# Performance work log

Hardware: AMD Instinct MI355X
Metric: run time of the kernel (lower is better)

Reference implementation:

```python
import jax, jax.numpy as jnp
import numpy as np

D_MODEL = 1024
H = 16
D_K = D_MODEL // H
D_FF = 4096
EPS = 1e-6
NEG = -1.0e9


def setup_inputs() -> dict:
    key = jax.random.key(0)
    ks = jax.random.split(key, 8)
    B, S = 4, 2048
    x = jax.random.normal(ks[0], (B, S, D_MODEL), dtype=jnp.float32)
    src_mask = jnp.ones((B, 1, S, S), dtype=jnp.int32)
    s = 0.02
    wq = jax.random.normal(ks[1], (D_MODEL, D_MODEL), jnp.float32) * s
    wk = jax.random.normal(ks[2], (D_MODEL, D_MODEL), jnp.float32) * s
    wv = jax.random.normal(ks[3], (D_MODEL, D_MODEL), jnp.float32) * s
    wo = jax.random.normal(ks[4], (D_MODEL, D_MODEL), jnp.float32) * s
    w1 = jax.random.normal(ks[5], (D_MODEL, D_FF), jnp.float32) * s
    b1 = jnp.zeros((D_FF,), jnp.float32)
    w2 = jax.random.normal(ks[6], (D_FF, D_MODEL), jnp.float32) * s
    b2 = jnp.zeros((D_MODEL,), jnp.float32)
    # LayerNorm params are scalars in the original (torch.ones(1)/zeros(1))
    a1 = jnp.ones((1,), jnp.float32); bt1 = jnp.zeros((1,), jnp.float32)
    a2 = jnp.ones((1,), jnp.float32); bt2 = jnp.zeros((1,), jnp.float32)
    return {"x": x, "src_mask": src_mask, "wq": wq, "wk": wk, "wv": wv,
            "wo": wo, "w1": w1, "b1": b1, "w2": w2, "b2": b2,
            "a1": a1, "bt1": bt1, "a2": a2, "bt2": bt2}


def _layernorm(x, alpha, beta):
    # Original: (x - mean) / (std + eps), std with Bessel correction (torch default)
    mean = jnp.mean(x, axis=-1, keepdims=True)
    std = jnp.std(x, axis=-1, keepdims=True, ddof=1)
    return alpha * (x - mean) / (std + EPS) + beta


def _mha(x, mask, wq, wk, wv, wo):
    B, S, _ = x.shape
    q = (x @ wq).reshape(B, S, H, D_K).transpose(0, 2, 1, 3)  # [B,H,S,Dk]
    k = (x @ wk).reshape(B, S, H, D_K).transpose(0, 2, 1, 3)
    v = (x @ wv).reshape(B, S, H, D_K).transpose(0, 2, 1, 3)
    scores = jnp.einsum('bhqd,bhkd->bhqk', q, k) / jnp.sqrt(jnp.float32(D_K))
    scores = jnp.where(mask == 0, NEG, scores)
    attn = jax.nn.softmax(scores, axis=-1)
    out = jnp.einsum('bhqk,bhkd->bhqd', attn, v)  # [B,H,S,Dk]
    out = out.transpose(0, 2, 1, 3).reshape(B, S, D_MODEL)
    return out @ wo


def reference(x, src_mask, wq, wk, wv, wo, w1, b1, w2, b2, a1, bt1, a2, bt2):
    # Sublayer 1: self-attention with post-norm residual (dropout = eval/identity)
    attn_out = _mha(x, src_mask, wq, wk, wv, wo)
    x = _layernorm(x + attn_out, a1, bt1)
    # Sublayer 2: FFN with post-norm residual
    ffn_out = jax.nn.relu(x @ w1 + b1) @ w2 + b2
    x = _layernorm(x + ffn_out, a2, bt2)
    return x
```

## Files before the change

kernel.cpp:

```cpp
#include <hip/hip_runtime.h>
#include <stdint.h>

typedef __bf16 bf16x8 __attribute__((ext_vector_type(8)));
typedef float f32x4 __attribute__((ext_vector_type(4)));
typedef unsigned short u16;
typedef u16 u16x8 __attribute__((ext_vector_type(8)));
typedef u16 u16x4 __attribute__((ext_vector_type(4)));
typedef uint32_t u32;

#define DEV __device__ __forceinline__
#define MFMA(a, b, c) __builtin_amdgcn_mfma_f32_16x16x32_bf16(a, b, c, 0, 0, 0)

static constexpr int B_ = 4, S_ = 2048, M_ = 8192, D_ = 1024, H_ = 16, DFF_ = 4096;

DEV u16 f2bf(float f) {
    union { float f; u32 u; } c; c.f = f;
    u32 u = c.u;
    return (u16)((u + 0x7fffu + ((u >> 16) & 1u)) >> 16);
}

DEV u32 cvt_pk_bf16(float lo, float hi) {
    u32 r;
    asm("v_cvt_pk_bf16_f32 %0, %1, %2" : "=v"(r) : "v"(lo), "v"(hi));
    return r;
}

DEV float v_exp2(float x) {
    float r;
    asm("v_exp_f32 %0, %1" : "=v"(r) : "v"(x));
    return r;
}

DEV void gload16(void* lds, const void* g) {
    __builtin_amdgcn_global_load_lds(
        (const __attribute__((address_space(1))) unsigned int*)g,
        (__attribute__((address_space(3))) unsigned int*)lds, 16, 0, 0);
}


__global__ __launch_bounds__(256) void k_pack_mask(const int* __restrict__ m,
                                                   u32* __restrict__ bits, int nwords) {
    int w = blockIdx.x * 256 + threadIdx.x;
    if (w >= nwords) return;
    const int4* s = (const int4*)(m + (size_t)w * 32);
    u32 r = 0;
#pragma unroll
    for (int j = 0; j < 8; j++) {
        int4 v = s[j];
        r |= (u32)(v.x != 0) << (j * 4) | (u32)(v.y != 0) << (j * 4 + 1) |
             (u32)(v.z != 0) << (j * 4 + 2) | (u32)(v.w != 0) << (j * 4 + 3);
    }
    bits[w] = r;
}

__global__ __launch_bounds__(256) void k_cast_bf16(const float* __restrict__ s,
                                                   u16* __restrict__ d, int n4) {
    int i = blockIdx.x * 256 + threadIdx.x;
    if (i >= n4) return;
    f32x4 v = ((const f32x4*)s)[i];
    u16x4 o;
    o[0] = f2bf(v[0]); o[1] = f2bf(v[1]); o[2] = f2bf(v[2]); o[3] = f2bf(v[3]);
    ((u16x4*)d)[i] = o;
}

__global__ void k_transpose_cast(const float* __restrict__ s, u16* __restrict__ d,
                                 int K, int N) {
    __shared__ float t[32][33];
    int n0 = blockIdx.x * 32, k0 = blockIdx.y * 32;
    int tx = threadIdx.x, ty = threadIdx.y;
#pragma unroll
    for (int i = 0; i < 4; i++)
        t[ty + i * 8][tx] = s[(size_t)(k0 + ty + i * 8) * N + n0 + tx];
    __syncthreads();
#pragma unroll
    for (int i = 0; i < 4; i++)
        d[(size_t)(n0 + ty + i * 8) * K + k0 + tx] = f2bf(t[tx][ty + i * 8]);
}

__global__ __launch_bounds__(256) void k_transpose_v(const u16* __restrict__ qkv,
                                                     u16* __restrict__ vT) {
    __shared__ u16 t[64][68];
    const int bh = blockIdx.y, s0 = blockIdx.x * 64;
    const int r = threadIdx.x >> 2, c = (threadIdx.x & 3) * 16;
    const u16* src = qkv + ((size_t)(128 + bh) * 2048 + s0 + r) * 64 + c;
    *(u16x8*)&t[r][c] = *(const u16x8*)src;
    *(u16x8*)&t[r][c + 8] = *(const u16x8*)(src + 8);
    __syncthreads();
    u16x8 o0, o1;
#pragma unroll
    for (int e = 0; e < 8; e++) { o0[e] = t[c + e][r]; o1[e] = t[c + 8 + e][r]; }
    u16* dst = vT + ((size_t)bh * 64 + r) * 2048 + s0 + c;
    *(u16x8*)dst = o0;
    *(u16x8*)(dst + 8) = o1;
}

template <int EPI>
__global__ __launch_bounds__(512, 2) void k_gemm256(const u16* __restrict__ A,
                                                    const u16* __restrict__ Bt,
                                                    float* __restrict__ Cf,
                                                    u16* __restrict__ Cb,
                                                    const float* __restrict__ bias,
                                                    int N, int K) {
    __shared__ u16 As[2][256 * 64];
    __shared__ u16 Bs[2][256 * 64];
    const int tid = threadIdx.x, lane = tid & 63, wave = tid >> 6;
    const int lr = lane & 15, lg = lane >> 4;
    const int wm = wave >> 2, wn = wave & 3;
    const int nbx = N >> 8;
    const int chunk = gridDim.x >> 3;
    const int id = ((int)blockIdx.x & 7) * chunk + ((int)blockIdx.x >> 3);
    const size_t row0 = (size_t)(id / nbx) * 256;
    const int col0 = (id % nbx) * 256;
    const int srow = lane >> 3;
    const int sgr = (lane & 7) ^ srow;
    const int NT = K >> 6;
    f32x4 acc[8][4] = {};

    auto stage_half = [&](int isB, int buf, int t, int h) {
        const u16* g = isB ? Bt : A;
        const size_t grow0 = isB ? (size_t)col0 : row0;
        char* base = isB ? (char*)&Bs[buf][0] : (char*)&As[buf][0];
#pragma unroll
        for (int l = 0; l < 2; l++) {
            int rt = h * 128 + l * 64 + wave * 8;
            gload16(base + rt * 128,
                    (const char*)(g + (grow0 + rt + srow) * K + t * 64 + sgr * 8));
        }
    };
    auto rdA = [&](int cur, int mh, int m, int kk) -> bf16x8 {
        int r = wm * 128 + mh * 64 + m * 16 + lr;
        int gi = kk * 4 + lg;
        return *(const bf16x8*)((char*)&As[cur][0] + r * 128 + ((gi ^ (r & 7)) << 4));
    };
    auto rdB = [&](int cur, int nh, int n, int kk) -> bf16x8 {
        int r = wn * 64 + nh * 32 + n * 16 + lr;
        int gi = kk * 4 + lg;
        return *(const bf16x8*)((char*)&Bs[cur][0] + r * 128 + ((gi ^ (r & 7)) << 4));
    };

    stage_half(0, 0, 0, 0); stage_half(0, 0, 0, 1);
    stage_half(1, 0, 0, 0); stage_half(1, 0, 0, 1);
    stage_half(1, 1, 1, 0); stage_half(1, 1, 1, 1);
    asm volatile("s_waitcnt vmcnt(4)" ::: "memory");
    __builtin_amdgcn_s_barrier();

    bf16x8 aF[4][2], b0F[2][2], b1F[2][2];
    for (int t = 0; t < NT; ++t) {
        const int cur = t & 1, nxt = cur ^ 1;
#pragma unroll
        for (int m = 0; m < 4; m++) { aF[m][0] = rdA(cur, 0, m, 0); aF[m][1] = rdA(cur, 0, m, 1); }
#pragma unroll
        for (int n = 0; n < 2; n++) { b0F[n][0] = rdB(cur, 0, n, 0); b0F[n][1] = rdB(cur, 0, n, 1); }
        if (t + 1 < NT) stage_half(0, nxt, t + 1, 0);
        __builtin_amdgcn_s_barrier();
        asm volatile("s_waitcnt lgkmcnt(0)" ::: "memory");
        __builtin_amdgcn_sched_barrier(0);
        __builtin_amdgcn_s_setprio(1);
#pragma unroll
        for (int m = 0; m < 4; m++)
#pragma unroll
            for (int n = 0; n < 2; n++) {
                acc[m][n] = MFMA(aF[m][0], b0F[n][0], acc[m][n]);
                acc[m][n] = MFMA(aF[m][1], b0F[n][1], acc[m][n]);
            }
        __builtin_amdgcn_s_setprio(0);
        __builtin_amdgcn_s_barrier();
#pragma unroll
        for (int n = 0; n < 2; n++) { b1F[n][0] = rdB(cur, 1, n, 0); b1F[n][1] = rdB(cur, 1, n, 1); }
        if (t + 1 < NT) stage_half(0, nxt, t + 1, 1);
        __builtin_amdgcn_s_barrier();
        asm volatile("s_waitcnt lgkmcnt(0)" ::: "memory");
        __builtin_amdgcn_sched_barrier(0);
        __builtin_amdgcn_s_setprio(1);
#pragma unroll
        for (int m = 0; m < 4; m++)
#pragma unroll
            for (int n = 0; n < 2; n++) {
                acc[m][2 + n] = MFMA(aF[m][0], b1F[n][0], acc[m][2 + n]);
                acc[m][2 + n] = MFMA(aF[m][1], b1F[n][1], acc[m][2 + n]);
            }
        __builtin_amdgcn_s_setprio(0);
        __builtin_amdgcn_s_barrier();
#pragma unroll
        for (int m = 0; m < 4; m++) { aF[m][0] = rdA(cur, 1, m, 0); aF[m][1] = rdA(cur, 1, m, 1); }
        if (t + 2 < NT) stage_half(1, cur, t + 2, 0);
        __builtin_amdgcn_s_barrier();
        asm volatile("s_waitcnt lgkmcnt(0)" ::: "memory");
        __builtin_amdgcn_sched_barrier(0);
        __builtin_amdgcn_s_setprio(1);
#pragma unroll
        for (int m = 0; m < 4; m++)
#pragma unroll
            for (int n = 0; n < 2; n++) {
                acc[4 + m][2 + n] = MFMA(aF[m][0], b1F[n][0], acc[4 + m][2 + n]);
                acc[4 + m][2 + n] = MFMA(aF[m][1], b1F[n][1], acc[4 + m][2 + n]);
            }
        __builtin_amdgcn_s_setprio(0);
        __builtin_amdgcn_s_barrier();
        if (t + 2 < NT) stage_half(1, cur, t + 2, 1);
        if (t + 1 < NT) {
            if (t + 2 < NT) asm volatile("s_waitcnt vmcnt(4)" ::: "memory");
            else            asm volatile("s_waitcnt vmcnt(0)" ::: "memory");
        }
        __builtin_amdgcn_s_barrier();
        __builtin_amdgcn_s_setprio(1);
#pragma unroll
        for (int m = 0; m < 4; m++)
#pragma unroll
            for (int n = 0; n < 2; n++) {
                acc[4 + m][n] = MFMA(aF[m][0], b0F[n][0], acc[4 + m][n]);
                acc[4 + m][n] = MFMA(aF[m][1], b0F[n][1], acc[4 + m][n]);
            }
        __builtin_amdgcn_s_setprio(0);
        __builtin_amdgcn_s_barrier();
    }
#pragma unroll
    for (int m = 0; m < 8; m++)
#pragma unroll
        for (int n = 0; n < 4; n++)
#pragma unroll
            for (int i = 0; i < 4; i++) {
                int rg = (int)row0 + wm * 128 + m * 16 + lg * 4 + i;
                int cg = col0 + wn * 64 + n * 16 + lr;
                float v = acc[m][n][i];
                if constexpr (EPI == 0) {
                    if (cg < 1024) v *= 0.1803368801111832f;
                    int proj = cg >> 10, hh = (cg >> 6) & 15, dk = cg & 63;
                    int b = rg >> 11, s = rg & 2047;
                    size_t idx = ((size_t)(proj * 64 + b * 16 + hh) * 2048 + s) * 64 + dk;
                    Cb[idx] = f2bf(v);
                } else if constexpr (EPI == 1) {
                    Cf[(size_t)rg * N + cg] = v;
                } else if constexpr (EPI == 2) {
                    v += bias[cg];
                    v = v > 0.f ? v : 0.f;
                    Cb[(size_t)rg * N + cg] = f2bf(v);
                } else {
                    Cf[(size_t)rg * N + cg] = v + bias[cg];
                }
            }
}

template <int EPI>
__global__ __launch_bounds__(512, 4) void k_gemm8(const u16* __restrict__ A,
                                                  const u16* __restrict__ Bt,
                                                  float* __restrict__ Cf,
                                                  u16* __restrict__ Cb,
                                                  const float* __restrict__ bias,
                                                  int N, int K) {
    __shared__ u16 As[2][128 * 64];
    __shared__ u16 Bs[2][128 * 64];
    const int tid = threadIdx.x, lane = tid & 63, wave = tid >> 6;
    const int lr = lane & 15, lg = lane >> 4;
    const int wm = wave >> 1, wn = wave & 1;
    const int nbx = N >> 7;
    const int chunk = gridDim.x >> 3;
    const int id = ((int)blockIdx.x & 7) * chunk + ((int)blockIdx.x >> 3);
    const size_t row0 = (size_t)(id / nbx) * 128;
    const int col0 = (id % nbx) * 128;
    const int srow = lane >> 3;
    const int sgr = (lane & 7) ^ srow;
    const int NT = K >> 6;
    f32x4 acc[2][4] = {};

    auto stage = [&](int buf, int t) {
#pragma unroll
        for (int i = 0; i < 2; i++) {
            int c = i * 8 + wave;
            gload16((char*)&As[buf][0] + c * 1024,
                    (const char*)(A + (row0 + c * 8 + srow) * K + t * 64 + sgr * 8));
        }
#pragma unroll
        for (int i = 0; i < 2; i++) {
            int c = i * 8 + wave;
            gload16((char*)&Bs[buf][0] + c * 1024,
                    (const char*)(Bt + (size_t)(col0 + c * 8 + srow) * K + t * 64 + sgr * 8));
        }
    };

    stage(0, 0);
    for (int t = 0; t < NT; ++t) {
        const int cur = t & 1;
        if (t + 1 < NT) {
            stage(cur ^ 1, t + 1);
            asm volatile("s_waitcnt vmcnt(4)" ::: "memory");
        } else {
            asm volatile("s_waitcnt vmcnt(0)" ::: "memory");
        }
        __builtin_amdgcn_s_barrier();
        asm volatile("" ::: "memory");
        bf16x8 bF[4][2];
#pragma unroll
        for (int n = 0; n < 4; n++) {
            int r = wn * 64 + n * 16 + lr;
            int rb = r * 128, sw = (r & 7) << 4;
#pragma unroll
            for (int ks = 0; ks < 2; ks++)
                bF[n][ks] = *(const bf16x8*)((char*)&Bs[cur][0] +
                                             (rb + ((ks * 64 + lg * 16) ^ sw)));
        }
#pragma unroll
        for (int m = 0; m < 2; m++) {
            int r = wm * 32 + m * 16 + lr;
            int rb = r * 128, sw = (r & 7) << 4;
            bf16x8 a0 = *(const bf16x8*)((char*)&As[cur][0] + (rb + ((lg * 16) ^ sw)));
            bf16x8 a1 = *(const bf16x8*)((char*)&As[cur][0] + (rb + ((64 + lg * 16) ^ sw)));
            __builtin_amdgcn_s_setprio(1);
#pragma unroll
            for (int n = 0; n < 4; n++) {
                acc[m][n] = MFMA(a0, bF[n][0], acc[m][n]);
                acc[m][n] = MFMA(a1, bF[n][1], acc[m][n]);
            }
            __builtin_amdgcn_s_setprio(0);
        }
        asm volatile("" ::: "memory");
        __builtin_amdgcn_s_barrier();
    }
#pragma unroll
    for (int m = 0; m < 2; m++)
#pragma unroll
        for (int n = 0; n < 4; n++)
#pragma unroll
            for (int i = 0; i < 4; i++) {
                int rg = (int)row0 + wm * 32 + m * 16 + lg * 4 + i;
                int cg = col0 + wn * 64 + n * 16 + lr;
                float v = acc[m][n][i];
                if constexpr (EPI == 0) {
                    if (cg < 1024) v *= 0.1803368801111832f;
                    int proj = cg >> 10, hh = (cg >> 6) & 15, dk = cg & 63;
                    int b = rg >> 11, s = rg & 2047;
                    size_t idx = ((size_t)(proj * 64 + b * 16 + hh) * 2048 + s) * 64 + dk;
                    Cb[idx] = f2bf(v);
                } else if constexpr (EPI == 1) {
                    Cf[(size_t)rg * N + cg] = v;
                } else if constexpr (EPI == 2) {
                    v += bias[cg];
                    v = v > 0.f ? v : 0.f;
                    Cb[(size_t)rg * N + cg] = f2bf(v);
                } else {
                    Cf[(size_t)rg * N + cg] = v + bias[cg];
                }
            }
}

__global__ __launch_bounds__(256) void k_attn(const u16* __restrict__ qkv,
                                              const u16* __restrict__ vT,
                                              const u32* __restrict__ mbits,
                                              u16* __restrict__ outb) {
    __shared__ u16 Kt[2][64 * 64];
    __shared__ u16 Vt[2][64 * 64];
    __shared__ u16 Pt[4][32 * 64];
    __shared__ u32 pm[2][128][2];
    const int tid = threadIdx.x, lane = tid & 63, wave = tid >> 6;
    const int lr = lane & 15, lg = lane >> 4;
    const int id0 = blockIdx.y * 16 + blockIdx.x;
    const int id = (id0 & 7) * 128 + (id0 >> 3);
    const int bh = id >> 4;
    const int b = bh >> 4, h = bh & 15;
    const int qb0 = (id & 15) * 128;
    const size_t qbase = (size_t)bh * (2048 * 64);
    const size_t kbase = (size_t)(64 + bh) * (2048 * 64);
    const size_t vtbase = (size_t)bh * (64 * 2048);

    bf16x8 qf[2][2];
    const int q0 = qb0 + wave * 32;
#pragma unroll
    for (int rs = 0; rs < 2; rs++)
#pragma unroll
        for (int kf = 0; kf < 2; kf++)
            qf[rs][kf] = *(const bf16x8*)(qkv + qbase +
                                          (size_t)(q0 + rs * 16 + lr) * 64 + kf * 32 + lg * 8);

    u16x8 ones_u;
#pragma unroll
    for (int e = 0; e < 8; e++) ones_u[e] = 0x3f80;
    const bf16x8 ones8 = *(const bf16x8*)&ones_u;

    f32x4 o[2][4] = {};
    f32x4 lacc[2] = {};
    const int str = tid >> 2, sq = tid & 3;
    const int swzs = (str & 7) << 4;
    const f32x4 zinit = {-16.f, -16.f, -16.f, -16.f};

    u16x8 krA, krB, vrA, vrB; u32 mwA;
    auto issue_loads = [&](int kv0n) {
        const u16* ksrc = qkv + kbase + (size_t)(kv0n + str) * 64 + sq * 16;
        krA = *(const u16x8*)ksrc; krB = *(const u16x8*)(ksrc + 8);
        const u16* vsrc = vT + vtbase + (size_t)str * 2048 + kv0n + sq * 16;
        vrA = *(const u16x8*)vsrc; vrB = *(const u16x8*)(vsrc + 8);
        mwA = mbits[(size_t)(b * 2048 + qb0 + (tid >> 1)) * 64 + (kv0n >> 5) + (tid & 1)];
    };
    auto write_tile = [&](int buf) -> bool {
        int b0 = str * 128 + sq * 32;
        *(u16x8*)((char*)&Kt[buf][0] + ((b0) ^ swzs)) = krA;
        *(u16x8*)((char*)&Kt[buf][0] + ((b0 + 16) ^ swzs)) = krB;
        *(u16x8*)((char*)&Vt[buf][0] + ((b0) ^ swzs)) = vrA;
        *(u16x8*)((char*)&Vt[buf][0] + ((b0 + 16) ^ swzs)) = vrB;
        pm[buf][tid >> 1][tid & 1] = mwA;
        return (__ballot(mwA == 0xffffffffu) == ~0ull);
    };

    issue_loads(0);
    bool aon_nxt = write_tile(0);
    for (int t = 0; t < 32; ++t) {
        const int cur = t & 1;
        const bool aon = aon_nxt ||
                         false;
        bool aon_cur = aon_nxt;
        if (t + 1 < 32) issue_loads((t + 1) * 64);
        asm volatile("s_waitcnt lgkmcnt(0)" ::: "memory");
        __builtin_amdgcn_s_barrier();
        (void)aon;

        f32x4 st[2][4];
#pragma unroll
        for (int ks = 0; ks < 4; ks++) {
            int rr = ks * 16 + lr;
            int rb = rr * 128, sw = (rr & 7) << 4;
            bf16x8 k0 = *(const bf16x8*)((char*)&Kt[cur][0] + ((rb + lg * 16) ^ sw));
            bf16x8 k1 = *(const bf16x8*)((char*)&Kt[cur][0] + ((rb + 64 + lg * 16) ^ sw));
#pragma unroll
            for (int rs = 0; rs < 2; rs++) {
                f32x4 z = MFMA(k0, qf[rs][0], zinit);
                z = MFMA(k1, qf[rs][1], z);
                st[rs][ks] = z;
            }
        }
        if (!aon_cur) {
#pragma unroll
            for (int rs = 0; rs < 2; rs++) {
                u32 w0 = pm[cur][wave * 32 + rs * 16 + lr][0];
                u32 w1 = pm[cur][wave * 32 + rs * 16 + lr][1];
#pragma unroll
                for (int ks = 0; ks < 4; ks++)
#pragma unroll
                    for (int i = 0; i < 4; i++) {
                        int kv = ks * 16 + lg * 4 + i;
                        u32 w = (kv & 32) ? w1 : w0;
                        if (!((w >> (kv & 31)) & 1u)) st[rs][ks][i] = -1e9f;
                    }
            }
        }
#pragma unroll
        for (int rs = 0; rs < 2; rs++) {
            int prow = rs * 16 + lr;
            int pb = prow * 128, swp = (prow & 7) << 4;
#pragma unroll
            for (int ks = 0; ks < 4; ks++) {
                uint2 w;
                w.x = cvt_pk_bf16(v_exp2(st[rs][ks][0]), v_exp2(st[rs][ks][1]));
                w.y = cvt_pk_bf16(v_exp2(st[rs][ks][2]), v_exp2(st[rs][ks][3]));
                *(uint2*)((char*)&Pt[wave][0] + ((pb + ks * 32 + lg * 8) ^ swp)) = w;
            }
        }
        asm volatile("s_waitcnt lgkmcnt(0)" ::: "memory");
        __builtin_amdgcn_sched_barrier(0);
        bf16x8 pf[2][2];
#pragma unroll
        for (int rs = 0; rs < 2; rs++) {
            int prow = rs * 16 + lr;
            int pb = prow * 128, swp = (prow & 7) << 4;
            pf[rs][0] = *(const bf16x8*)((char*)&Pt[wave][0] + ((pb + lg * 16) ^ swp));
            pf[rs][1] = *(const bf16x8*)((char*)&Pt[wave][0] + ((pb + 64 + lg * 16) ^ swp));
        }
#pragma unroll
        for (int rs = 0; rs < 2; rs++) {
            lacc[rs] = MFMA(ones8, pf[rs][0], lacc[rs]);
            lacc[rs] = MFMA(ones8, pf[rs][1], lacc[rs]);
        }
#pragma unroll
        for (int ns = 0; ns < 4; ns++) {
            int vr = ns * 16 + lr;
            int vb = vr * 128, sw = (vr & 7) << 4;
            bf16x8 v0 = *(const bf16x8*)((char*)&Vt[cur][0] + ((vb + lg * 16) ^ sw));
            bf16x8 v1 = *(const bf16x8*)((char*)&Vt[cur][0] + ((vb + 64 + lg * 16) ^ sw));
#pragma unroll
            for (int rs = 0; rs < 2; rs++) {
                o[rs][ns] = MFMA(v0, pf[rs][0], o[rs][ns]);
                o[rs][ns] = MFMA(v1, pf[rs][1], o[rs][ns]);
            }
        }
        if (t + 1 < 32) aon_nxt = write_tile(cur ^ 1);
    }
#pragma unroll
    for (int rs = 0; rs < 2; rs++) {
        float inv = 1.f / lacc[rs][0];
        int qg = qb0 + wave * 32 + rs * 16 + lr;
#pragma unroll
        for (int ns = 0; ns < 4; ns++) {
            u16x4 ov;
#pragma unroll
            for (int i = 0; i < 4; i++) ov[i] = f2bf(o[rs][ns][i] * inv);
            *(u16x4*)(outb + (size_t)(b * 2048 + qg) * 1024 + h * 64 + ns * 16 + lg * 4) = ov;
        }
    }
}

template <bool WB>
__global__ __launch_bounds__(256) void k_add_ln(const float* __restrict__ y,
                                                const float* __restrict__ resid,
                                                float* __restrict__ outf,
                                                u16* __restrict__ outb,
                                                const float* __restrict__ alpha,
                                                const float* __restrict__ beta) {
    const int row = blockIdx.x, tid = threadIdx.x;
    const f32x4 a = ((const f32x4*)(y + (size_t)row * 1024))[tid];
    const f32x4 r = ((const f32x4*)(resid + (size_t)row * 1024))[tid];
    f32x4 t;
#pragma unroll
    for (int i = 0; i < 4; i++) t[i] = a[i] + r[i];
    float s = t[0] + t[1] + t[2] + t[3];
    float ss = t[0] * t[0] + t[1] * t[1] + t[2] * t[2] + t[3] * t[3];
#pragma unroll
    for (int m2 = 1; m2 < 64; m2 <<= 1) {
        s += __shfl_xor(s, m2);
        ss += __shfl_xor(ss, m2);
    }
    __shared__ float ps[4], pss[4];
    if ((tid & 63) == 0) { ps[tid >> 6] = s; pss[tid >> 6] = ss; }
    __syncthreads();
    s = ps[0] + ps[1] + ps[2] + ps[3];
    ss = pss[0] + pss[1] + pss[2] + pss[3];
    const float mean = s * (1.f / 1024.f);
    float var = (ss - 1024.f * mean * mean) * (1.f / 1023.f);
    var = fmaxf(var, 0.f);
    const float inv = alpha[0] / (sqrtf(var) + 1e-6f);
    const float bet = beta[0];
    f32x4 oo;
#pragma unroll
    for (int i = 0; i < 4; i++) oo[i] = (t[i] - mean) * inv + bet;
    ((f32x4*)(outf + (size_t)row * 1024))[tid] = oo;
    if constexpr (WB) {
        u16x4 ob;
#pragma unroll
        for (int i = 0; i < 4; i++) ob[i] = f2bf(oo[i]);
        ((u16x4*)(outb + (size_t)row * 1024))[tid] = ob;
    }
}

extern "C" void kernel_launch(void* const* d_in, const int* in_sizes, int n_in,
                              void* d_out, int out_size, void* d_ws, size_t ws_size,
                              hipStream_t stream) {
    const float* x   = (const float*)d_in[0];
    const int*   msk = (const int*)d_in[1];
    const float* wq  = (const float*)d_in[2];
    const float* wk  = (const float*)d_in[3];
    const float* wv  = (const float*)d_in[4];
    const float* wo  = (const float*)d_in[5];
    const float* w1  = (const float*)d_in[6];
    const float* b1  = (const float*)d_in[7];
    const float* w2  = (const float*)d_in[8];
    const float* b2  = (const float*)d_in[9];
    const float* a1  = (const float*)d_in[10];
    const float* bt1 = (const float*)d_in[11];
    const float* a2  = (const float*)d_in[12];
    const float* bt2 = (const float*)d_in[13];
    float* out = (float*)d_out;

    char* ws = (char*)d_ws;
    size_t off = 0;
    auto alloc = [&](size_t bytes) {
        void* p = ws + off;
        off += (bytes + 255) & ~(size_t)255;
        return p;
    };
    u16* xb    = (u16*)alloc((size_t)M_ * D_ * 2);
    u16* wqkvT = (u16*)alloc((size_t)3 * D_ * D_ * 2);
    u16* woT   = (u16*)alloc((size_t)D_ * D_ * 2);
    u16* w1T   = (u16*)alloc((size_t)DFF_ * D_ * 2);
    u16* w2T   = (u16*)alloc((size_t)D_ * DFF_ * 2);
    u32* mbits = (u32*)alloc((size_t)B_ * S_ * 64 * 4);
    u16* aout  = (u16*)alloc((size_t)M_ * D_ * 2);
    float* y   = (float*)alloc((size_t)M_ * D_ * 4);
    float* x1  = (float*)alloc((size_t)M_ * D_ * 4);
    u16* x1b   = (u16*)alloc((size_t)M_ * D_ * 2);
    u16* vTb   = (u16*)alloc((size_t)64 * 64 * 2048 * 2);
    u16* qkv   = (u16*)alloc((size_t)M_ * DFF_ * 2);
    u16* hft   = qkv;

    k_pack_mask<<<dim3((B_ * S_ * 64) / 256), 256, 0, stream>>>(msk, mbits, B_ * S_ * 64);
    k_cast_bf16<<<dim3((M_ * D_ / 4) / 256), 256, 0, stream>>>(x, xb, M_ * D_ / 4);
    dim3 tb(32, 8);
    k_transpose_cast<<<dim3(32, 32), tb, 0, stream>>>(wq, wqkvT, D_, D_);
    k_transpose_cast<<<dim3(32, 32), tb, 0, stream>>>(wk, wqkvT + D_ * D_, D_, D_);
    k_transpose_cast<<<dim3(32, 32), tb, 0, stream>>>(wv, wqkvT + 2 * D_ * D_, D_, D_);
    k_transpose_cast<<<dim3(32, 32), tb, 0, stream>>>(wo, woT, D_, D_);
    k_transpose_cast<<<dim3(128, 32), tb, 0, stream>>>(w1, w1T, D_, DFF_);
    k_transpose_cast<<<dim3(32, 128), tb, 0, stream>>>(w2, w2T, DFF_, D_);

    k_gemm256<0><<<dim3(384), 512, 0, stream>>>(xb, wqkvT, nullptr, qkv, nullptr,
                                                3 * D_, D_);
    k_transpose_v<<<dim3(32, 64), 256, 0, stream>>>(qkv, vTb);
    k_attn<<<dim3(16, 64), 256, 0, stream>>>(qkv, vTb, mbits, aout);
    k_gemm8<1><<<dim3(512), 512, 0, stream>>>(aout, woT, y, nullptr, nullptr, D_, D_);
    k_add_ln<true><<<dim3(M_), 256, 0, stream>>>(y, x, x1, x1b, a1, bt1);
    k_gemm256<2><<<dim3(512), 512, 0, stream>>>(x1b, w1T, nullptr, hft, b1, DFF_, D_);
    k_gemm8<3><<<dim3(512), 512, 0, stream>>>(hft, w2T, y, nullptr, b2, D_, DFF_);
    k_add_ln<false><<<dim3(M_), 256, 0, stream>>>(y, x1, out, nullptr, a2, bt2);
}
```

Measured before the change: 420.1 us.

## Fuse V transpose into QKV GEMM epilogue and residual adds into GEMMs

The QKV projection moves from the 256-tile GEMM to the 128-tile GEMM, whose epilogue now writes V directly in transposed layout, so the separate V transpose kernel is dropped. The residual additions move from the LayerNorm kernels into the output-projection and FFN2 GEMM epilogues, and LayerNorm now reads a single pre-summed input. The goal is to cut extra passes over global memory and one kernel launch. The cost is that the QKV GEMM runs with smaller tiles, giving more blocks and lower per-block reuse, and the transposed V stores are strided 8-byte writes.

```diff
diff --git a/kernel.cpp b/kernel.cpp
--- a/kernel.cpp
+++ b/kernel.cpp
@@ -77,21 +77,121 @@
         d[(size_t)(n0 + ty + i * 8) * K + k0 + tx] = f2bf(t[tx][ty + i * 8]);
 }
 
-__global__ __launch_bounds__(256) void k_transpose_v(const u16* __restrict__ qkv,
-                                                     u16* __restrict__ vT) {
-    __shared__ u16 t[64][68];
-    const int bh = blockIdx.y, s0 = blockIdx.x * 64;
-    const int r = threadIdx.x >> 2, c = (threadIdx.x & 3) * 16;
-    const u16* src = qkv + ((size_t)(128 + bh) * 2048 + s0 + r) * 64 + c;
-    *(u16x8*)&t[r][c] = *(const u16x8*)src;
-    *(u16x8*)&t[r][c + 8] = *(const u16x8*)(src + 8);
-    __syncthreads();
-    u16x8 o0, o1;
-#pragma unroll
-    for (int e = 0; e < 8; e++) { o0[e] = t[c + e][r]; o1[e] = t[c + 8 + e][r]; }
-    u16* dst = vT + ((size_t)bh * 64 + r) * 2048 + s0 + c;
-    *(u16x8*)dst = o0;
-    *(u16x8*)(dst + 8) = o1;
+template <int EPI>
+__global__ __launch_bounds__(512, 4) void k_gemm8(const u16* __restrict__ A,
+                                                  const u16* __restrict__ Bt,
+                                                  float* __restrict__ Cf,
+                                                  u16* __restrict__ Cb,
+                                                  const float* __restrict__ bias,
+                                                  const float* __restrict__ resid,
+                                                  u16* __restrict__ Vt,
+                                                  int N, int K) {
+    __shared__ u16 As[2][128 * 64];
+    __shared__ u16 Bs[2][128 * 64];
+    const int tid = threadIdx.x, lane = tid & 63, wave = tid >> 6;
+    const int lr = lane & 15, lg = lane >> 4;
+    const int wm = wave >> 1, wn = wave & 1;
+    const int nbx = N >> 7;
+    const int chunk = gridDim.x >> 3;
+    const int id = ((int)blockIdx.x & 7) * chunk + ((int)blockIdx.x >> 3);
+    const size_t row0 = (size_t)(id / nbx) * 128;
+    const int col0 = (id % nbx) * 128;
+    const int srow = lane >> 3;
+    const int sgr = (lane & 7) ^ srow;
+    const int NT = K >> 6;
+    f32x4 acc[2][4] = {};
+
+    auto stage = [&](int buf, int t) {
+#pragma unroll
+        for (int i = 0; i < 2; i++) {
+            int c = i * 8 + wave;
+            gload16((char*)&As[buf][0] + c * 1024,
+                    (const char*)(A + (row0 + c * 8 + srow) * K + t * 64 + sgr * 8));
+        }
+#pragma unroll
+        for (int i = 0; i < 2; i++) {
+            int c = i * 8 + wave;
+            gload16((char*)&Bs[buf][0] + c * 1024,
+                    (const char*)(Bt + (size_t)(col0 + c * 8 + srow) * K + t * 64 + sgr * 8));
+        }
+    };
+
+    stage(0, 0);
+    for (int t = 0; t < NT; ++t) {
+        const int cur = t & 1;
+        if (t + 1 < NT) {
+            stage(cur ^ 1, t + 1);
+            asm volatile("s_waitcnt vmcnt(4)" ::: "memory");
+        } else {
+            asm volatile("s_waitcnt vmcnt(0)" ::: "memory");
+        }
+        __builtin_amdgcn_s_barrier();
+        asm volatile("" ::: "memory");
+        bf16x8 bF[4][2];
+#pragma unroll
+        for (int n = 0; n < 4; n++) {
+            int r = wn * 64 + n * 16 + lr;
+            int rb = r * 128, sw = (r & 7) << 4;
+#pragma unroll
+            for (int ks = 0; ks < 2; ks++)
+                bF[n][ks] = *(const bf16x8*)((char*)&Bs[cur][0] +
+                                             (rb + ((ks * 64 + lg * 16) ^ sw)));
+        }
+#pragma unroll
+        for (int m = 0; m < 2; m++) {
+            int r = wm * 32 + m * 16 + lr;
+            int rb = r * 128, sw = (r & 7) << 4;
+            bf16x8 a0 = *(const bf16x8*)((char*)&As[cur][0] + (rb + ((lg * 16) ^ sw)));
+            bf16x8 a1 = *(const bf16x8*)((char*)&As[cur][0] + (rb + ((64 + lg * 16) ^ sw)));
+            __builtin_amdgcn_s_setprio(1);
+#pragma unroll
+            for (int n = 0; n < 4; n++) {
+                acc[m][n] = MFMA(a0, bF[n][0], acc[m][n]);
+                acc[m][n] = MFMA(a1, bF[n][1], acc[m][n]);
+            }
+            __builtin_amdgcn_s_setprio(0);
+        }
+        asm volatile("" ::: "memory");
+        __builtin_amdgcn_s_barrier();
+    }
+#pragma unroll
+    for (int m = 0; m < 2; m++)
+#pragma unroll
+        for (int n = 0; n < 4; n++) {
+            const int cg = col0 + wn * 64 + n * 16 + lr;
+            const int rbase = (int)row0 + wm * 32 + m * 16 + lg * 4;
+            if constexpr (EPI == 0) {
+                const int proj = cg >> 10, hh = (cg >> 6) & 15, dk = cg & 63;
+                const int b = rbase >> 11, s = rbase & 2047;
+                if (proj == 2) {
+                    u16x4 ov;
+#pragma unroll
+                    for (int i = 0; i < 4; i++) ov[i] = f2bf(acc[m][n][i]);
+                    *(u16x4*)(Vt + ((size_t)(b * 16 + hh) * 64 + dk) * 2048 + s) = ov;
+                } else {
+                    const float sc = (proj == 0) ? 0.1803368801111832f : 1.f;
+                    size_t base = ((size_t)(proj * 64 + b * 16 + hh) * 2048 + s) * 64 + dk;
+#pragma unroll
+                    for (int i = 0; i < 4; i++)
+                        Cb[base + (size_t)i * 64] = f2bf(acc[m][n][i] * sc);
+                }
+            } else {
+#pragma unroll
+                for (int i = 0; i < 4; i++) {
+                    const int rg = rbase + i;
+                    float v = acc[m][n][i];
+                    if constexpr (EPI == 1) {
+                        Cf[(size_t)rg * N + cg] = v + resid[(size_t)rg * N + cg];
+                    } else if constexpr (EPI == 2) {
+                        v += bias[cg];
+                        v = v > 0.f ? v : 0.f;
+                        Cb[(size_t)rg * N + cg] = f2bf(v);
+                    } else {
+                        Cf[(size_t)rg * N + cg] = v + bias[cg] + resid[(size_t)rg * N + cg];
+                    }
+                }
+            }
+        }
 }
 
 template <int EPI>
@@ -223,122 +323,12 @@
                 int rg = (int)row0 + wm * 128 + m * 16 + lg * 4 + i;
                 int cg = col0 + wn * 64 + n * 16 + lr;
                 float v = acc[m][n][i];
-                if constexpr (EPI == 0) {
-                    if (cg < 1024) v *= 0.1803368801111832f;
-                    int proj = cg >> 10, hh = (cg >> 6) & 15, dk = cg & 63;
-                    int b = rg >> 11, s = rg & 2047;
-                    size_t idx = ((size_t)(proj * 64 + b * 16 + hh) * 2048 + s) * 64 + dk;
-                    Cb[idx] = f2bf(v);
-                } else if constexpr (EPI == 1) {
-                    Cf[(size_t)rg * N + cg] = v;
-                } else if constexpr (EPI == 2) {
+                if constexpr (EPI == 2) {
                     v += bias[cg];
                     v = v > 0.f ? v : 0.f;
                     Cb[(size_t)rg * N + cg] = f2bf(v);
                 } else {
-                    Cf[(size_t)rg * N + cg] = v + bias[cg];
-                }
-            }
-}
-
-template <int EPI>
-__global__ __launch_bounds__(512, 4) void k_gemm8(const u16* __restrict__ A,
-                                                  const u16* __restrict__ Bt,
-                                                  float* __restrict__ Cf,
-                                                  u16* __restrict__ Cb,
-                                                  const float* __restrict__ bias,
-                                                  int N, int K) {
-    __shared__ u16 As[2][128 * 64];
-    __shared__ u16 Bs[2][128 * 64];
-    const int tid = threadIdx.x, lane = tid & 63, wave = tid >> 6;
-    const int lr = lane & 15, lg = lane >> 4;
-    const int wm = wave >> 1, wn = wave & 1;
-    const int nbx = N >> 7;
-    const int chunk = gridDim.x >> 3;
-    const int id = ((int)blockIdx.x & 7) * chunk + ((int)blockIdx.x >> 3);
-    const size_t row0 = (size_t)(id / nbx) * 128;
-    const int col0 = (id % nbx) * 128;
-    const int srow = lane >> 3;
-    const int sgr = (lane & 7) ^ srow;
-    const int NT = K >> 6;
-    f32x4 acc[2][4] = {};
-
-    auto stage = [&](int buf, int t) {
-#pragma unroll
-        for (int i = 0; i < 2; i++) {
-            int c = i * 8 + wave;
-            gload16((char*)&As[buf][0] + c * 1024,
-                    (const char*)(A + (row0 + c * 8 + srow) * K + t * 64 + sgr * 8));
-        }
-#pragma unroll
-        for (int i = 0; i < 2; i++) {
-            int c = i * 8 + wave;
-            gload16((char*)&Bs[buf][0] + c * 1024,
-                    (const char*)(Bt + (size_t)(col0 + c * 8 + srow) * K + t * 64 + sgr * 8));
-        }
-    };
-
-    stage(0, 0);
-    for (int t = 0; t < NT; ++t) {
-        const int cur = t & 1;
-        if (t + 1 < NT) {
-            stage(cur ^ 1, t + 1);
-            asm volatile("s_waitcnt vmcnt(4)" ::: "memory");
-        } else {
-            asm volatile("s_waitcnt vmcnt(0)" ::: "memory");
-        }
-        __builtin_amdgcn_s_barrier();
-        asm volatile("" ::: "memory");
-        bf16x8 bF[4][2];
-#pragma unroll
-        for (int n = 0; n < 4; n++) {
-            int r = wn * 64 + n * 16 + lr;
-            int rb = r * 128, sw = (r & 7) << 4;
-#pragma unroll
-            for (int ks = 0; ks < 2; ks++)
-                bF[n][ks] = *(const bf16x8*)((char*)&Bs[cur][0] +
-                                             (rb + ((ks * 64 + lg * 16) ^ sw)));
-        }
-#pragma unroll
-        for (int m = 0; m < 2; m++) {
-            int r = wm * 32 + m * 16 + lr;
-            int rb = r * 128, sw = (r & 7) << 4;
-            bf16x8 a0 = *(const bf16x8*)((char*)&As[cur][0] + (rb + ((lg * 16) ^ sw)));
-            bf16x8 a1 = *(const bf16x8*)((char*)&As[cur][0] + (rb + ((64 + lg * 16) ^ sw)));
-            __builtin_amdgcn_s_setprio(1);
-#pragma unroll
-            for (int n = 0; n < 4; n++) {
-                acc[m][n] = MFMA(a0, bF[n][0], acc[m][n]);
-                acc[m][n] = MFMA(a1, bF[n][1], acc[m][n]);
-            }
-            __builtin_amdgcn_s_setprio(0);
-        }
-        asm volatile("" ::: "memory");
-        __builtin_amdgcn_s_barrier();
-    }
-#pragma unroll
-    for (int m = 0; m < 2; m++)
-#pragma unroll
-        for (int n = 0; n < 4; n++)
-#pragma unroll
-            for (int i = 0; i < 4; i++) {
-                int rg = (int)row0 + wm * 32 + m * 16 + lg * 4 + i;
-                int cg = col0 + wn * 64 + n * 16 + lr;
-                float v = acc[m][n][i];
-                if constexpr (EPI == 0) {
-                    if (cg < 1024) v *= 0.1803368801111832f;
-                    int proj = cg >> 10, hh = (cg >> 6) & 15, dk = cg & 63;
-                    int b = rg >> 11, s = rg & 2047;
-                    size_t idx = ((size_t)(proj * 64 + b * 16 + hh) * 2048 + s) * 64 + dk;
-                    Cb[idx] = f2bf(v);
-                } else if constexpr (EPI == 1) {
                     Cf[(size_t)rg * N + cg] = v;
-                } else if constexpr (EPI == 2) {
-                    v += bias[cg];
-                    v = v > 0.f ? v : 0.f;
-                    Cb[(size_t)rg * N + cg] = f2bf(v);
-                } else {
-                    Cf[(size_t)rg * N + cg] = v + bias[cg];
                 }
             }
 }
@@ -404,13 +394,10 @@
     bool aon_nxt = write_tile(0);
     for (int t = 0; t < 32; ++t) {
         const int cur = t & 1;
-        const bool aon = aon_nxt ||
-                         false;
-        bool aon_cur = aon_nxt;
+        const bool aon_cur = aon_nxt;
         if (t + 1 < 32) issue_loads((t + 1) * 64);
         asm volatile("s_waitcnt lgkmcnt(0)" ::: "memory");
         __builtin_amdgcn_s_barrier();
-        (void)aon;
 
         f32x4 st[2][4];
 #pragma unroll
@@ -497,18 +484,13 @@
 }
 
 template <bool WB>
-__global__ __launch_bounds__(256) void k_add_ln(const float* __restrict__ y,
-                                                const float* __restrict__ resid,
-                                                float* __restrict__ outf,
-                                                u16* __restrict__ outb,
-                                                const float* __restrict__ alpha,
-                                                const float* __restrict__ beta) {
+__global__ __launch_bounds__(256) void k_ln(const float* __restrict__ tin,
+                                            float* __restrict__ outf,
+                                            u16* __restrict__ outb,
+                                            const float* __restrict__ alpha,
+                                            const float* __restrict__ beta) {
     const int row = blockIdx.x, tid = threadIdx.x;
-    const f32x4 a = ((const f32x4*)(y + (size_t)row * 1024))[tid];
-    const f32x4 r = ((const f32x4*)(resid + (size_t)row * 1024))[tid];
-    f32x4 t;
-#pragma unroll
-    for (int i = 0; i < 4; i++) t[i] = a[i] + r[i];
+    const f32x4 t = ((const f32x4*)(tin + (size_t)row * 1024))[tid];
     float s = t[0] + t[1] + t[2] + t[3];
     float ss = t[0] * t[0] + t[1] * t[1] + t[2] * t[2] + t[3] * t[3];
 #pragma unroll
@@ -588,13 +570,14 @@
     k_transpose_cast<<<dim3(128, 32), tb, 0, stream>>>(w1, w1T, D_, DFF_);
     k_transpose_cast<<<dim3(32, 128), tb, 0, stream>>>(w2, w2T, DFF_, D_);
 
-    k_gemm256<0><<<dim3(384), 512, 0, stream>>>(xb, wqkvT, nullptr, qkv, nullptr,
-                                                3 * D_, D_);
-    k_transpose_v<<<dim3(32, 64), 256, 0, stream>>>(qkv, vTb);
+    k_gemm8<0><<<dim3(1536), 512, 0, stream>>>(xb, wqkvT, nullptr, qkv, nullptr,
+                                               nullptr, vTb, 3 * D_, D_);
     k_attn<<<dim3(16, 64), 256, 0, stream>>>(qkv, vTb, mbits, aout);
-    k_gemm8<1><<<dim3(512), 512, 0, stream>>>(aout, woT, y, nullptr, nullptr, D_, D_);
-    k_add_ln<true><<<dim3(M_), 256, 0, stream>>>(y, x, x1, x1b, a1, bt1);
+    k_gemm8<1><<<dim3(512), 512, 0, stream>>>(aout, woT, y, nullptr, nullptr, x,
+                                              nullptr, D_, D_);
+    k_ln<true><<<dim3(M_), 256, 0, stream>>>(y, x1, x1b, a1, bt1);
     k_gemm256<2><<<dim3(512), 512, 0, stream>>>(x1b, w1T, nullptr, hft, b1, DFF_, D_);
-    k_gemm8<3><<<dim3(512), 512, 0, stream>>>(hft, w2T, y, nullptr, b2, D_, DFF_);
-    k_add_ln<false><<<dim3(M_), 256, 0, stream>>>(y, x1, out, nullptr, a2, bt2);
-}
+    k_gemm8<3><<<dim3(512), 512, 0, stream>>>(hft, w2T, y, nullptr, b2, x1,
+                                              nullptr, D_, DFF_);
+    k_ln<false><<<dim3(M_), 256, 0, stream>>>(y, out, nullptr, a2, bt2);
+}
```

Result: no change. 412.7 us (-1.8%).
